# Performance work log

Hardware: AMD Instinct MI355X
Metric: run time of the kernel (lower is better)

## Reference

```python
import jax, jax.numpy as jnp
import numpy as np

L, N, E, H = 1024, 8, 1024, 16
D = E // H

def setup_inputs() -> dict:
    key = jax.random.key(0)
    k1, k2, k3 = jax.random.split(key, 3)
    x = jax.random.normal(k1, (L, N, E), dtype=jnp.float32)
    # xavier-uniform-like scale for in_proj_weight (3E x E)
    bound = float(np.sqrt(6.0 / (3 * E + E)))
    in_proj_weight = jax.random.uniform(k2, (3 * E, E), dtype=jnp.float32, minval=-bound, maxval=bound)
    in_proj_bias = jnp.zeros((3 * E,), dtype=jnp.float32)
    wb = float(np.sqrt(1.0 / E))
    out_w = jax.random.uniform(k3, (E, E), dtype=jnp.float32, minval=-wb, maxval=wb)
    out_b = jnp.zeros((E,), dtype=jnp.float32)
    return {"x": x, "in_proj_weight": in_proj_weight, "in_proj_bias": in_proj_bias,
            "out_w": out_w, "out_b": out_b}

def reference(x, in_proj_weight, in_proj_bias, out_w, out_b):
    # self-attention: query == key == value == x, stacked input projection
    stack = x @ in_proj_weight.T + in_proj_bias          # L x N x 3E
    q, k, v = jnp.split(stack, 3, axis=-1)               # each L x N x E
    q = q.reshape(L, N, H, D)
    k = k.reshape(L, N, H, D)
    v = v.reshape(L, N, H, D)
    logit = jnp.einsum('lnhd,snhd->lnhs', q, k) / jnp.sqrt(jnp.float32(D))
    weight = jax.nn.softmax(logit, axis=-1)              # L x N x H x S
    context = jnp.einsum('lnhs,snhd->lnhd', weight, v)   # L x N x H x D
    context = context.reshape(L, N, E) @ out_w.T + out_b # L x N x E
    attn = jnp.transpose(weight.mean(axis=-2), (1, 0, 2))  # N x L x S
    return context, attn
```

## Files before the change

kernel.cpp:

```cpp
#include <hip/hip_runtime.h>
#include <stdint.h>

#define LL 1024
#define NB 8
#define EE 1024
#define HH 16
#define DD 64
#define MM (LL*NB)
#define K3 (3*EE)

typedef __attribute__((ext_vector_type(8))) short bf16x8;
typedef __attribute__((ext_vector_type(4))) float f32x4;
typedef __attribute__((ext_vector_type(4))) unsigned short u16x4;
typedef __attribute__((ext_vector_type(8))) unsigned short u16x8;

__device__ __forceinline__ unsigned short f2bf(float f) {
  uint32_t u = __builtin_bit_cast(uint32_t, f);
  u += 0x7fffu + ((u >> 16) & 1u);
  return (unsigned short)(u >> 16);
}
__device__ __forceinline__ uint32_t cvtpk(float lo, float hi) {
  uint32_t d;
  asm volatile("v_cvt_pk_bf16_f32 %0, %1, %2" : "=v"(d) : "v"(lo), "v"(hi));
  return d;
}
__device__ __forceinline__ f32x4 mfma16(bf16x8 a, bf16x8 b, f32x4 c) {
  return __builtin_amdgcn_mfma_f32_16x16x32_bf16(a, b, c, 0, 0, 0);
}
__device__ __forceinline__ void gload16(const unsigned short* src, unsigned short* dst) {
  __builtin_amdgcn_global_load_lds(
      (const __attribute__((address_space(1))) uint32_t*)src,
      (__attribute__((address_space(3))) uint32_t*)dst, 16, 0, 0);
}

__global__ void cvt3_kernel(const float* __restrict__ a, const float* __restrict__ b,
                            const float* __restrict__ c,
                            unsigned short* __restrict__ da, unsigned short* __restrict__ db,
                            unsigned short* __restrict__ dc) {
  const int NA = (MM * EE) / 4, NBq = (K3 * EE) / 4, NC = (EE * EE) / 4;
  const int total = NA + NBq + NC;
  for (int i = blockIdx.x * blockDim.x + threadIdx.x; i < total; i += gridDim.x * blockDim.x) {
    const float* s; unsigned short* d; int j;
    if (i < NA)            { s = a; d = da; j = i; }
    else if (i < NA + NBq) { s = b; d = db; j = i - NA; }
    else                   { s = c; d = dc; j = i - NA - NBq; }
    f32x4 v = ((const f32x4*)s)[j];
    u16x4 o;
    o[0] = f2bf(v[0]); o[1] = f2bf(v[1]); o[2] = f2bf(v[2]); o[3] = f2bf(v[3]);
    ((u16x4*)d)[j] = o;
  }
}

template<int MODE>
__global__ __launch_bounds__(256, 2) void gemm_bt(
    const unsigned short* __restrict__ A, const unsigned short* __restrict__ B,
    const float* __restrict__ bias, float* __restrict__ Cf,
    unsigned short* __restrict__ qo, unsigned short* __restrict__ kto,
    unsigned short* __restrict__ vo)
{
  constexpr int NNc = (MODE == 1) ? 3072 : 1024;
  constexpr int BPC = NNc / 256;
  constexpr int KD  = 1024;
  constexpr int SMEM = (MODE == 1) ? 33280 : 24576;
  __shared__ __align__(16) unsigned short smem[SMEM];

  const int bid = blockIdx.x;
  const int q8 = gridDim.x >> 3;
  const int wgid = (bid & 7) * q8 + (bid >> 3);
  const int brow = wgid / BPC;
  const int bcol = wgid % BPC;

  const int tid = threadIdx.x;
  const int w = tid >> 6, lane = tid & 63;
  const int wr = w >> 1, wc = w & 1;
  const int lrow = lane & 15, g = lane >> 4;

  f32x4 acc[4][8];
#pragma unroll
  for (int i = 0; i < 4; ++i)
#pragma unroll
    for (int j = 0; j < 8; ++j) acc[i][j] = (f32x4){0.f, 0.f, 0.f, 0.f};

  const int r_in = lane >> 2;
  const int u = lane & 3;

  auto stage = [&](int kt) {
    unsigned short* base = smem + ((kt & 1) ? 12288 : 0);
    unsigned short* a_lds = base;
    unsigned short* b_lds = base + 4096;
    const size_t kcol = (size_t)kt * 32 + u * 8;
    gload16(A + (size_t)(brow * 128 + 16 * w + r_in) * KD + kcol,       &a_lds[(16 * w) * 32]);
    gload16(A + (size_t)(brow * 128 + 16 * (w + 4) + r_in) * KD + kcol, &a_lds[(16 * (w + 4)) * 32]);
#pragma unroll
    for (int i = 0; i < 4; ++i)
      gload16(B + (size_t)(bcol * 256 + 16 * (w + 4 * i) + r_in) * KD + kcol,
              &b_lds[(16 * (w + 4 * i)) * 32]);
  };

  const int KT = KD >> 5;
  stage(0);
  for (int kt = 0; kt < KT; ++kt) {
    __syncthreads();
    if (kt + 1 < KT) stage(kt + 1);
    const unsigned short* base = smem + ((kt & 1) ? 12288 : 0);
    const unsigned short* a_lds = base;
    const unsigned short* b_lds = base + 4096;
    bf16x8 af[4], bfr[8];
#pragma unroll
    for (int mt = 0; mt < 4; ++mt)
      af[mt] = *(const bf16x8*)&a_lds[(wr * 64 + mt * 16 + lrow) * 32 + g * 8];
#pragma unroll
    for (int nt = 0; nt < 8; ++nt)
      bfr[nt] = *(const bf16x8*)&b_lds[(wc * 128 + nt * 16 + lrow) * 32 + g * 8];
#pragma unroll
    for (int mt = 0; mt < 4; ++mt)
#pragma unroll
      for (int nt = 0; nt < 8; ++nt)
        acc[mt][nt] = mfma16(af[mt], bfr[nt], acc[mt][nt]);
  }

  if (MODE == 0) {
#pragma unroll
    for (int nt = 0; nt < 8; ++nt) {
      const int c = bcol * 256 + wc * 128 + nt * 16 + lrow;
      const float bv = bias[c];
#pragma unroll
      for (int mt = 0; mt < 4; ++mt) {
        const int m0 = brow * 128 + wr * 64 + mt * 16 + g * 4;
#pragma unroll
        for (int j = 0; j < 4; ++j)
          Cf[(size_t)(m0 + j) * NNc + c] = acc[mt][nt][j] + bv;
      }
    }
  } else {
    __syncthreads();
    const float qs = (bcol < 4) ? 0.125f : 1.0f;
#pragma unroll
    for (int nt = 0; nt < 8; ++nt) {
      const int c = bcol * 256 + wc * 128 + nt * 16 + lrow;
      const float bv = bias[c];
      const int lc = wc * 128 + nt * 16 + lrow;
#pragma unroll
      for (int mt = 0; mt < 4; ++mt) {
        const int lr0 = wr * 64 + mt * 16 + g * 4;
#pragma unroll
        for (int j = 0; j < 4; ++j)
          smem[(lr0 + j) * 260 + lc] = f2bf((acc[mt][nt][j] + bv) * qs);
      }
    }
    __syncthreads();
#pragma unroll
    for (int i = 0; i < 16; ++i) {
      const int unit = i * 256 + tid;
      const int r = unit >> 5, cu = unit & 31;
      const u16x8 val = *(const u16x8*)&smem[r * 260 + cu * 8];
      const int m = brow * 128 + r;
      const int c = bcol * 256 + cu * 8;
      const int region = c >> 10, cl = c & 1023;
      if (region == 0)      *(u16x8*)&qo[(size_t)m * EE + cl] = val;
      else if (region == 2) *(u16x8*)&vo[(size_t)m * EE + cl] = val;
      else *(u16x8*)&kto[((size_t)((m & 7) * HH + (cl >> 6)) * LL + (m >> 3)) * DD + (cl & 63)] = val;
    }
  }
}

__global__ void transpose_v(const unsigned short* __restrict__ v, unsigned short* __restrict__ vt) {
  __shared__ __align__(16) unsigned short tile[64][68];
  const int b = blockIdx.x;
  const int lchunk = b & 15, h = (b >> 4) & 15, n = b >> 8;
  const int t = threadIdx.x;
  const int c4 = (t & 15) * 4, r = t >> 4;
#pragma unroll
  for (int p = 0; p < 4; ++p) {
    const int l = lchunk * 64 + p * 16 + r;
    u16x4 x = *(const u16x4*)&v[(size_t)(l * NB + n) * EE + h * DD + c4];
    *(u16x4*)&tile[p * 16 + r][c4] = x;
  }
  __syncthreads();
#pragma unroll
  for (int p = 0; p < 4; ++p) {
    const int d = p * 16 + r;
    u16x4 o;
#pragma unroll
    for (int i = 0; i < 4; ++i) o[i] = tile[c4 + i][d];
    *(u16x4*)&vt[((size_t)(n * HH + h) * DD + d) * LL + lchunk * 64 + c4] = o;
  }
}

__global__ __launch_bounds__(256) void attn_flash(
    const unsigned short* __restrict__ q,
    const unsigned short* __restrict__ kt,
    const unsigned short* __restrict__ vt,
    unsigned short* __restrict__ ctxo,
    float* __restrict__ rinvb)
{
  __shared__ __align__(16) unsigned short kc[2][64][64];
  __shared__ __align__(16) unsigned short pl[4][4][16][72];

  const int bid = blockIdx.x;
  const int n = bid & 7;
  const int rest = bid >> 3;
  const int h = rest >> 2;
  const int lt = (rest & 3) << 8;
  const int tid = threadIdx.x;
  const int wv = tid >> 6, lane = tid & 63;
  const int ll = lane & 15, g = lane >> 4;
  const int a3 = ll & 7;

  bf16x8 qf0[4], qf1[4];
#pragma unroll
  for (int T = 0; T < 4; ++T) {
    const int lr = lt + T * 64 + wv * 16 + ll;
    const unsigned short* qp = q + ((size_t)lr * NB + n) * EE + h * DD + g * 8;
    qf0[T] = *(const bf16x8*)qp;
    qf1[T] = *(const bf16x8*)(qp + 32);
  }

  const unsigned short* kslab = kt + (size_t)(n * HH + h) * LL * DD;
  const unsigned short* vbase = vt + (size_t)(n * HH + h) * DD * LL;

  const int r8 = lane >> 3;
  const int c16 = (lane & 7) ^ r8;
  const int kof0 = ll * 128 + ((g ^ a3) << 4);
  const int kof1 = ll * 128 + (((4 + g) ^ a3) << 4);

  auto stageK = [&](int buf, int ch) {
    unsigned short* kd = &kc[buf][wv * 16][0];
    const unsigned short* src = kslab + (size_t)(ch * 64 + wv * 16) * DD;
    gload16(src + (size_t)r8 * DD + c16 * 8,       kd);
    gload16(src + (size_t)(8 + r8) * DD + c16 * 8, kd + 8 * 64);
  };

  f32x4 ctx[4][4];
  f32x4 sum[4];
#pragma unroll
  for (int T = 0; T < 4; ++T) {
    sum[T] = (f32x4){0.f, 0.f, 0.f, 0.f};
#pragma unroll
    for (int dt = 0; dt < 4; ++dt) ctx[T][dt] = (f32x4){0.f, 0.f, 0.f, 0.f};
  }

  char* plb = (char*)&pl[wv][0][0][0];

  stageK(0, 0);
  for (int ch = 0; ch < 16; ++ch) {
    __syncthreads();
    const int buf = ch & 1;
    const char* kb = (const char*)&kc[buf][0][0];

    bf16x8 vf0[4], vf1[4];
#pragma unroll
    for (int dt = 0; dt < 4; ++dt) {
      const unsigned short* vp = vbase + (size_t)(dt * 16 + ll) * LL + ch * 64 + g * 8;
      vf0[dt] = *(const bf16x8*)vp;
      vf1[dt] = *(const bf16x8*)(vp + 32);
    }
    if (ch < 15) stageK(buf ^ 1, ch + 1);

#pragma unroll
    for (int t = 0; t < 4; ++t) {
      const bf16x8 kf0 = *(const bf16x8*)(kb + t * 2048 + kof0);
      const bf16x8 kf1 = *(const bf16x8*)(kb + t * 2048 + kof1);
#pragma unroll
      for (int T = 0; T < 4; ++T) {
        f32x4 sc = (f32x4){0.f, 0.f, 0.f, 0.f};
        sc = mfma16(kf0, qf0[T], sc);
        sc = mfma16(kf1, qf1[T], sc);
        f32x4 p;
#pragma unroll
        for (int j = 0; j < 4; ++j) p[j] = __expf(sc[j]);
        sum[T] += p;
        uint2 wT; wT.x = cvtpk(p[0], p[1]); wT.y = cvtpk(p[2], p[3]);
        *(uint2*)(plb + T * 2304 + ll * 144 + (t * 16 + g * 4) * 2) = wT;
      }
    }
#pragma unroll
    for (int T = 0; T < 4; ++T) {
      const bf16x8 pf0 = *(const bf16x8*)(plb + T * 2304 + ll * 144 + g * 16);
      const bf16x8 pf1 = *(const bf16x8*)(plb + T * 2304 + ll * 144 + 64 + g * 16);
#pragma unroll
      for (int dt = 0; dt < 4; ++dt) {
        ctx[T][dt] = mfma16(vf0[dt], pf0, ctx[T][dt]);
        ctx[T][dt] = mfma16(vf1[dt], pf1, ctx[T][dt]);
      }
    }
  }

#pragma unroll
  for (int T = 0; T < 4; ++T) {
    float s1 = sum[T][0] + sum[T][1] + sum[T][2] + sum[T][3];
    s1 += __shfl_xor(s1, 16); s1 += __shfl_xor(s1, 32);
    const float rinv = 1.0f / s1;
    if (lane < 16) rinvb[(size_t)(n * HH + h) * LL + lt + T * 64 + wv * 16 + lane] = rinv;
    const int lr = lt + T * 64 + wv * 16 + ll;
    unsigned short* cp = ctxo + ((size_t)lr * NB + n) * EE + h * DD;
#pragma unroll
    for (int dt = 0; dt < 4; ++dt) {
      uint2 o;
      o.x = cvtpk(ctx[T][dt][0] * rinv, ctx[T][dt][1] * rinv);
      o.y = cvtpk(ctx[T][dt][2] * rinv, ctx[T][dt][3] * rinv);
      *(uint2*)(cp + dt * 16 + g * 4) = o;
    }
  }
}

__global__ __launch_bounds__(256) void attn_mean(
    const unsigned short* __restrict__ q,
    const unsigned short* __restrict__ kt,
    const float* __restrict__ rinvb,
    float* __restrict__ attn_out)
{
  __shared__ __align__(16) unsigned short kc[2][128][64];

  const int bid = blockIdx.x;
  const int n = bid & 7;
  const int r = bid >> 3;
  const int sh = r & 7;
  const int lt = (r >> 3) << 6;
  const int tid = threadIdx.x;
  const int wv = tid >> 6, lane = tid & 63;
  const int ll = lane & 15, g = lane >> 4;
  const int a3 = ll & 7;
  const int sb = sh << 7;
  const int lrow = lt + wv * 16 + ll;

  const int r8 = lane >> 3;
  const int c16 = (lane & 7) ^ r8;
  const int kof0 = ll * 128 + ((g ^ a3) << 4);
  const int kof1 = ll * 128 + (((4 + g) ^ a3) << 4);

  const unsigned short* kwin = kt + (size_t)n * HH * LL * DD + (size_t)sb * DD;

  auto stage = [&](int buf, int h) {
    unsigned short* kd = &kc[buf][wv * 32][0];
    const unsigned short* src = kwin + (size_t)h * LL * DD + (size_t)(wv * 32) * DD;
#pragma unroll
    for (int i = 0; i < 4; ++i)
      gload16(src + (size_t)(i * 8 + r8) * DD + c16 * 8, kd + i * 8 * 64);
  };

  float rv[16];
#pragma unroll
  for (int h = 0; h < HH; ++h) rv[h] = rinvb[(size_t)(n * HH + h) * LL + lrow];

  const unsigned short* qb2 = q + ((size_t)lrow * NB + n) * EE + g * 8;

  f32x4 acc[8];
#pragma unroll
  for (int i = 0; i < 8; ++i) acc[i] = (f32x4){0.f, 0.f, 0.f, 0.f};

  stage(0, 0);
  for (int h = 0; h < HH; ++h) {
    __syncthreads();
    const char* kb = (const char*)&kc[h & 1][0][0];
    const unsigned short* qp = qb2 + h * DD;
    const bf16x8 qf0 = *(const bf16x8*)qp;
    const bf16x8 qf1 = *(const bf16x8*)(qp + 32);
    if (h + 1 < HH) stage((h + 1) & 1, h + 1);
    const float rvh = rv[h];
#pragma unroll
    for (int t = 0; t < 8; ++t) {
      bf16x8 kf0 = *(const bf16x8*)(kb + t * 2048 + kof0);
      bf16x8 kf1 = *(const bf16x8*)(kb + t * 2048 + kof1);
      f32x4 sc = (f32x4){0.f, 0.f, 0.f, 0.f};
      sc = mfma16(kf0, qf0, sc);
      sc = mfma16(kf1, qf1, sc);
#pragma unroll
      for (int j = 0; j < 4; ++j) acc[t][j] += __expf(sc[j]) * rvh;
    }
  }

  float* ap = attn_out + ((size_t)n * LL + lrow) * LL + sb + g * 4;
#pragma unroll
  for (int t = 0; t < 8; ++t) *(f32x4*)(ap + t * 16) = acc[t] * 0.0625f;
}

extern "C" void kernel_launch(void* const* d_in, const int* in_sizes, int n_in,
                              void* d_out, int out_size, void* d_ws, size_t ws_size,
                              hipStream_t stream) {
  const float* x   = (const float*)d_in[0];
  const float* win = (const float*)d_in[1];
  const float* bin = (const float*)d_in[2];
  const float* ow  = (const float*)d_in[3];
  const float* ob  = (const float*)d_in[4];
  float* out = (float*)d_out;

  const size_t need = ((size_t)MM * EE * 5 + (size_t)K3 * EE + (size_t)EE * EE) * 2
                    + (size_t)NB * HH * LL * 4;
  if (ws_size < need) return;

  unsigned short* ws  = (unsigned short*)d_ws;
  unsigned short* xb  = ws;
  unsigned short* wb  = xb + (size_t)MM * EE;
  unsigned short* owb = wb + (size_t)K3 * EE;
  unsigned short* qb  = owb + (size_t)EE * EE;
  unsigned short* ktb = qb + (size_t)MM * EE;
  unsigned short* vb  = ktb + (size_t)MM * EE;
  unsigned short* vtb = vb + (size_t)MM * EE;
  float* rinvb = (float*)(vtb + (size_t)MM * EE);
  unsigned short* ctx = xb;

  cvt3_kernel<<<2048, 256, 0, stream>>>(x, win, ow, xb, wb, owb);
  gemm_bt<1><<<64 * (K3 / 256), 256, 0, stream>>>(xb, wb, bin, nullptr, qb, ktb, vb);
  transpose_v<<<2048, 256, 0, stream>>>(vb, vtb);
  attn_flash<<<512, 256, 0, stream>>>(qb, ktb, vtb, ctx, rinvb);
  attn_mean<<<1024, 256, 0, stream>>>(qb, ktb, rinvb, out + (size_t)MM * EE);
  gemm_bt<0><<<64 * (EE / 256), 256, 0, stream>>>(ctx, owb, ob, out, nullptr, nullptr, nullptr);
}
```

Before: 203.6 us.

## Replace QKV projection GEMM with 256x256-tile 8-wave kernel using direct-to-LDS loads

The stacked input projection GEMM now uses a new kernel with 512 threads, 256x256 output tiles and K-steps of 64. It stages tiles with direct global-to-LDS loads into an XOR-swizzled double buffer, interleaves the next tile's loads with MFMA groups and raises wave priority during the MFMA bursts. The larger tile is meant to raise data reuse per LDS byte and hide global latency better. In exchange it uses 128 KB of LDS per block, so occupancy drops, and the epilogue is done in two halves. The output-projection GEMM is split out as a non-templated copy of the old kernel.

Result: no change. 201.9 us (-0.8%).

```diff
diff --git a/kernel.cpp b/kernel.cpp
--- a/kernel.cpp
+++ b/kernel.cpp
@@ -51,24 +51,184 @@
   }
 }
 
-template<int MODE>
-__global__ __launch_bounds__(256, 2) void gemm_bt(
+__global__ __launch_bounds__(512, 2) void gemm8p(
     const unsigned short* __restrict__ A, const unsigned short* __restrict__ B,
-    const float* __restrict__ bias, float* __restrict__ Cf,
+    const float* __restrict__ bias,
     unsigned short* __restrict__ qo, unsigned short* __restrict__ kto,
     unsigned short* __restrict__ vo)
 {
-  constexpr int NNc = (MODE == 1) ? 3072 : 1024;
-  constexpr int BPC = NNc / 256;
-  constexpr int KD  = 1024;
-  constexpr int SMEM = (MODE == 1) ? 33280 : 24576;
-  __shared__ __align__(16) unsigned short smem[SMEM];
+  __shared__ __align__(16) unsigned short smem[65536];
+
+  const int bid = blockIdx.x;
+  const int wgid = (bid & 7) * 48 + (bid >> 3);
+  const int brow = wgid / 12;
+  const int bcol = wgid % 12;
+
+  const int tid = threadIdx.x;
+  const int w = tid >> 6, lane = tid & 63;
+  const int wm = w >> 2, wn = w & 3;
+  const int ll = lane & 15, g = lane >> 4;
+  const int a3 = ll & 7;
+  const int r8l = lane >> 3;
+  const int su = (lane & 7) ^ r8l;
+
+  const int kof0 = ll * 128 + ((g ^ a3) << 4);
+  const int kof1 = ll * 128 + (((4 + g) ^ a3) << 4);
+
+  auto issue = [&](int ktt, int s) {
+    const int nb = ktt & 1;
+    const bool isA = (s < 4);
+    const int i = isA ? s : s - 4;
+    unsigned short* dst = smem + nb * 32768 + (isA ? 0 : 16384) + (64 * i + 8 * w) * 64;
+    const unsigned short* src =
+        (isA ? A + (size_t)(brow * 256 + 64 * i + 8 * w + r8l) * 1024
+             : B + (size_t)(bcol * 256 + 64 * i + 8 * w + r8l) * 1024)
+        + ktt * 64 + su * 8;
+    gload16(src, dst);
+  };
+
+  f32x4 acc[8][4];
+#pragma unroll
+  for (int i = 0; i < 8; ++i)
+#pragma unroll
+    for (int j = 0; j < 4; ++j) acc[i][j] = (f32x4){0.f, 0.f, 0.f, 0.f};
+
+#pragma unroll
+  for (int s = 0; s < 8; ++s) issue(0, s);
+
+  for (int kt = 0; kt < 16; ++kt) {
+    const char* Ab = (const char*)(smem + (kt & 1) * 32768) + (wm * 128) * 128;
+    const char* Bb = (const char*)(smem + (kt & 1) * 32768 + 16384) + (wn * 64) * 128;
+
+    if (kt < 15) {
+      issue(kt + 1, 0); issue(kt + 1, 1);
+      asm volatile("s_waitcnt vmcnt(2)" ::: "memory");
+    } else {
+      asm volatile("s_waitcnt vmcnt(0)" ::: "memory");
+    }
+    __builtin_amdgcn_s_barrier();
+    __builtin_amdgcn_sched_barrier(0);
+
+    bf16x8 bf[4][2];
+#pragma unroll
+    for (int nt = 0; nt < 4; ++nt) {
+      bf[nt][0] = *(const bf16x8*)(Bb + nt * 2048 + kof0);
+      bf[nt][1] = *(const bf16x8*)(Bb + nt * 2048 + kof1);
+    }
+    {
+      bf16x8 a0k0 = *(const bf16x8*)(Ab + 0 * 2048 + kof0);
+      bf16x8 a0k1 = *(const bf16x8*)(Ab + 0 * 2048 + kof1);
+      bf16x8 a1k0 = *(const bf16x8*)(Ab + 1 * 2048 + kof0);
+      bf16x8 a1k1 = *(const bf16x8*)(Ab + 1 * 2048 + kof1);
+      __builtin_amdgcn_s_setprio(1);
+#pragma unroll
+      for (int nt = 0; nt < 4; ++nt) {
+        acc[0][nt] = mfma16(a0k0, bf[nt][0], acc[0][nt]);
+        acc[0][nt] = mfma16(a0k1, bf[nt][1], acc[0][nt]);
+        acc[1][nt] = mfma16(a1k0, bf[nt][0], acc[1][nt]);
+        acc[1][nt] = mfma16(a1k1, bf[nt][1], acc[1][nt]);
+      }
+      __builtin_amdgcn_s_setprio(0);
+    }
+    if (kt < 15) { issue(kt + 1, 2); issue(kt + 1, 3); }
+    {
+      bf16x8 a0k0 = *(const bf16x8*)(Ab + 2 * 2048 + kof0);
+      bf16x8 a0k1 = *(const bf16x8*)(Ab + 2 * 2048 + kof1);
+      bf16x8 a1k0 = *(const bf16x8*)(Ab + 3 * 2048 + kof0);
+      bf16x8 a1k1 = *(const bf16x8*)(Ab + 3 * 2048 + kof1);
+      __builtin_amdgcn_s_setprio(1);
+#pragma unroll
+      for (int nt = 0; nt < 4; ++nt) {
+        acc[2][nt] = mfma16(a0k0, bf[nt][0], acc[2][nt]);
+        acc[2][nt] = mfma16(a0k1, bf[nt][1], acc[2][nt]);
+        acc[3][nt] = mfma16(a1k0, bf[nt][0], acc[3][nt]);
+        acc[3][nt] = mfma16(a1k1, bf[nt][1], acc[3][nt]);
+      }
+      __builtin_amdgcn_s_setprio(0);
+    }
+    if (kt < 15) { issue(kt + 1, 4); issue(kt + 1, 5); }
+    {
+      bf16x8 a0k0 = *(const bf16x8*)(Ab + 4 * 2048 + kof0);
+      bf16x8 a0k1 = *(const bf16x8*)(Ab + 4 * 2048 + kof1);
+      bf16x8 a1k0 = *(const bf16x8*)(Ab + 5 * 2048 + kof0);
+      bf16x8 a1k1 = *(const bf16x8*)(Ab + 5 * 2048 + kof1);
+      __builtin_amdgcn_s_setprio(1);
+#pragma unroll
+      for (int nt = 0; nt < 4; ++nt) {
+        acc[4][nt] = mfma16(a0k0, bf[nt][0], acc[4][nt]);
+        acc[4][nt] = mfma16(a0k1, bf[nt][1], acc[4][nt]);
+        acc[5][nt] = mfma16(a1k0, bf[nt][0], acc[5][nt]);
+        acc[5][nt] = mfma16(a1k1, bf[nt][1], acc[5][nt]);
+      }
+      __builtin_amdgcn_s_setprio(0);
+    }
+    if (kt < 15) { issue(kt + 1, 6); issue(kt + 1, 7); }
+    {
+      bf16x8 a0k0 = *(const bf16x8*)(Ab + 6 * 2048 + kof0);
+      bf16x8 a0k1 = *(const bf16x8*)(Ab + 6 * 2048 + kof1);
+      bf16x8 a1k0 = *(const bf16x8*)(Ab + 7 * 2048 + kof0);
+      bf16x8 a1k1 = *(const bf16x8*)(Ab + 7 * 2048 + kof1);
+      __builtin_amdgcn_s_setprio(1);
+#pragma unroll
+      for (int nt = 0; nt < 4; ++nt) {
+        acc[6][nt] = mfma16(a0k0, bf[nt][0], acc[6][nt]);
+        acc[6][nt] = mfma16(a0k1, bf[nt][1], acc[6][nt]);
+        acc[7][nt] = mfma16(a1k0, bf[nt][0], acc[7][nt]);
+        acc[7][nt] = mfma16(a1k1, bf[nt][1], acc[7][nt]);
+      }
+      __builtin_amdgcn_s_setprio(0);
+    }
+    __builtin_amdgcn_sched_barrier(0);
+    __builtin_amdgcn_s_barrier();
+  }
+
+  const int region = bcol >> 2;
+  const float qs = (region == 0) ? 0.125f : 1.0f;
+#pragma unroll
+  for (int half = 0; half < 2; ++half) {
+    if (wm == half) {
+#pragma unroll
+      for (int nt = 0; nt < 4; ++nt) {
+        const int c = bcol * 256 + wn * 64 + nt * 16 + ll;
+        const float bv = bias[c];
+        const int lc = wn * 64 + nt * 16 + ll;
+#pragma unroll
+        for (int mt = 0; mt < 8; ++mt) {
+          const int lr0 = mt * 16 + g * 4;
+#pragma unroll
+          for (int j = 0; j < 4; ++j)
+            smem[(lr0 + j) * 260 + lc] = f2bf((acc[mt][nt][j] + bv) * qs);
+        }
+      }
+    }
+    __syncthreads();
+#pragma unroll
+    for (int it = 0; it < 8; ++it) {
+      const int unit = it * 512 + tid;
+      const int r = unit >> 5, cu = unit & 31;
+      const u16x8 val = *(const u16x8*)&smem[r * 260 + cu * 8];
+      const int m = brow * 256 + half * 128 + r;
+      const int cl = (bcol & 3) * 256 + cu * 8;
+      if (region == 0)      *(u16x8*)&qo[(size_t)m * EE + cl] = val;
+      else if (region == 2) *(u16x8*)&vo[(size_t)m * EE + cl] = val;
+      else *(u16x8*)&kto[((size_t)((m & 7) * HH + (cl >> 6)) * LL + (m >> 3)) * DD + (cl & 63)] = val;
+    }
+    __syncthreads();
+  }
+}
+
+__global__ __launch_bounds__(256, 2) void gemm_out(
+    const unsigned short* __restrict__ A, const unsigned short* __restrict__ B,
+    const float* __restrict__ bias, float* __restrict__ Cf)
+{
+  constexpr int KD = 1024;
+  __shared__ __align__(16) unsigned short smem[24576];
 
   const int bid = blockIdx.x;
   const int q8 = gridDim.x >> 3;
   const int wgid = (bid & 7) * q8 + (bid >> 3);
-  const int brow = wgid / BPC;
-  const int bcol = wgid % BPC;
+  const int brow = wgid >> 2;
+  const int bcol = wgid & 3;
 
   const int tid = threadIdx.x;
   const int w = tid >> 6, lane = tid & 63;
@@ -119,47 +279,16 @@
         acc[mt][nt] = mfma16(af[mt], bfr[nt], acc[mt][nt]);
   }
 
-  if (MODE == 0) {
-#pragma unroll
-    for (int nt = 0; nt < 8; ++nt) {
-      const int c = bcol * 256 + wc * 128 + nt * 16 + lrow;
-      const float bv = bias[c];
-#pragma unroll
-      for (int mt = 0; mt < 4; ++mt) {
-        const int m0 = brow * 128 + wr * 64 + mt * 16 + g * 4;
-#pragma unroll
-        for (int j = 0; j < 4; ++j)
-          Cf[(size_t)(m0 + j) * NNc + c] = acc[mt][nt][j] + bv;
-      }
-    }
-  } else {
-    __syncthreads();
-    const float qs = (bcol < 4) ? 0.125f : 1.0f;
-#pragma unroll
-    for (int nt = 0; nt < 8; ++nt) {
-      const int c = bcol * 256 + wc * 128 + nt * 16 + lrow;
-      const float bv = bias[c];
-      const int lc = wc * 128 + nt * 16 + lrow;
-#pragma unroll
-      for (int mt = 0; mt < 4; ++mt) {
-        const int lr0 = wr * 64 + mt * 16 + g * 4;
-#pragma unroll
-        for (int j = 0; j < 4; ++j)
-          smem[(lr0 + j) * 260 + lc] = f2bf((acc[mt][nt][j] + bv) * qs);
-      }
-    }
-    __syncthreads();
-#pragma unroll
-    for (int i = 0; i < 16; ++i) {
-      const int unit = i * 256 + tid;
-      const int r = unit >> 5, cu = unit & 31;
-      const u16x8 val = *(const u16x8*)&smem[r * 260 + cu * 8];
-      const int m = brow * 128 + r;
-      const int c = bcol * 256 + cu * 8;
-      const int region = c >> 10, cl = c & 1023;
-      if (region == 0)      *(u16x8*)&qo[(size_t)m * EE + cl] = val;
-      else if (region == 2) *(u16x8*)&vo[(size_t)m * EE + cl] = val;
-      else *(u16x8*)&kto[((size_t)((m & 7) * HH + (cl >> 6)) * LL + (m >> 3)) * DD + (cl & 63)] = val;
+#pragma unroll
+  for (int nt = 0; nt < 8; ++nt) {
+    const int c = bcol * 256 + wc * 128 + nt * 16 + lrow;
+    const float bv = bias[c];
+#pragma unroll
+    for (int mt = 0; mt < 4; ++mt) {
+      const int m0 = brow * 128 + wr * 64 + mt * 16 + g * 4;
+#pragma unroll
+      for (int j = 0; j < 4; ++j)
+        Cf[(size_t)(m0 + j) * 1024 + c] = acc[mt][nt][j] + bv;
     }
   }
 }
@@ -401,9 +530,9 @@
   unsigned short* ctx = xb;
 
   cvt3_kernel<<<2048, 256, 0, stream>>>(x, win, ow, xb, wb, owb);
-  gemm_bt<1><<<64 * (K3 / 256), 256, 0, stream>>>(xb, wb, bin, nullptr, qb, ktb, vb);
+  gemm8p<<<384, 512, 0, stream>>>(xb, wb, bin, qb, ktb, vb);
   transpose_v<<<2048, 256, 0, stream>>>(vb, vtb);
   attn_flash<<<512, 256, 0, stream>>>(qb, ktb, vtb, ctx, rinvb);
   attn_mean<<<1024, 256, 0, stream>>>(qb, ktb, rinvb, out + (size_t)MM * EE);
-  gemm_bt<0><<<64 * (EE / 256), 256, 0, stream>>>(ctx, owb, ob, out, nullptr, nullptr, nullptr);
-}
+  gemm_out<<<256, 256, 0, stream>>>(ctx, owb, ob, out);
+}
```
